# Kernel optimization log

Measured on AMD Instinct MI355X. Metric: run time of the kernel, lower is better.

The kernel has to match this reference:

```python
import jax, jax.numpy as jnp
import numpy as np

N_NODES = 50000
N_EDGES = 1600000
IN_DIM = 6
HID = 128
OUT = 128
N_LAYERS = 3
N_EXPERTS = 4
N_GRAPHS = 16
LOGN_SCALE = float(np.log(1e4))  # normalizes log(graph size) into ~[0,1]


def setup_inputs() -> dict:
    key = jax.random.key(0)
    ks = jax.random.split(key, 10)
    x = jax.random.normal(ks[0], (N_NODES, IN_DIM), dtype=jnp.float32)
    edge_index = jax.random.randint(ks[1], (2, N_EDGES), 0, N_NODES, dtype=jnp.int64)
    batch = jnp.sort(jax.random.randint(ks[2], (N_NODES,), 0, N_GRAPHS, dtype=jnp.int64))
    s = 1.0 / np.sqrt(HID)
    W_enc = jax.random.normal(ks[3], (IN_DIM, HID), dtype=jnp.float32) / np.sqrt(IN_DIM)
    b_enc = jnp.zeros((HID,), dtype=jnp.float32)
    # per-expert, per-layer GraphConv weights (hidden->hidden ... hidden->out; dims equal here)
    W_self = jax.random.normal(ks[4], (N_EXPERTS, N_LAYERS, HID, OUT), dtype=jnp.float32) * s
    W_nbr = jax.random.normal(ks[5], (N_EXPERTS, N_LAYERS, HID, OUT), dtype=jnp.float32) * s
    b_conv = jnp.zeros((N_EXPERTS, N_LAYERS, OUT), dtype=jnp.float32)
    centers = jnp.linspace(0.0, 1.0, N_EXPERTS, dtype=jnp.float32)
    return {"x": x, "edge_index": edge_index, "batch": batch, "W_enc": W_enc,
            "b_enc": b_enc, "W_self": W_self, "W_nbr": W_nbr, "b_conv": b_conv,
            "centers": centers}


def _expert(h, src, dst, Ws, Wn, b):
    # Ws, Wn: [L, H, H]; b: [L, H]
    for l in range(N_LAYERS):
        agg = jax.ops.segment_sum(h[src], dst, num_segments=N_NODES)  # gather+scatter
        h = h @ Ws[l] + agg @ Wn[l] + b[l]
        if l < N_LAYERS - 1:
            h = jax.nn.relu(h)
    return h


def reference(x, edge_index, batch, W_enc, b_enc, W_self, W_nbr, b_conv, centers):
    src, dst = edge_index[0], edge_index[1]
    h = jax.nn.relu(x @ W_enc + b_enc)  # SharedBusEncoder
    # graph size features: normalized log(#nodes per graph), per node
    counts = jax.ops.segment_sum(jnp.ones((N_NODES,), jnp.float32), batch,
                                 num_segments=N_GRAPHS)
    logn = jnp.log(jnp.maximum(counts, 1.0))[batch] / LOGN_SCALE  # [N]
    probs = jax.nn.softmax(-(logn[:, None] - centers[None, :]) ** 2, axis=-1)  # [N, E]
    y = jax.vmap(_expert, in_axes=(None, None, None, 0, 0, 0))(
        h, src, dst, W_self, W_nbr, b_conv)  # [E, N, OUT]
    return jnp.einsum('enh,ne->nh', y, probs)
```

## Files before the change

kernel.cpp:

```cpp
#include <hip/hip_runtime.h>

#define NN 50000
#define NE 1600000
#define NG 16
#define HID 128
#define NEXP 4
#define LOGN_SCALE 9.210340371976184f

#define NBUK 256
#define NPB  196
#define NBLK 128
#define EPB  ((NE + NBLK - 1)/NBLK)
#define MAXB 16384

typedef unsigned short u16;
typedef unsigned int u32;
typedef unsigned char u8;
typedef __attribute__((ext_vector_type(8))) short short8b;
typedef __attribute__((ext_vector_type(4))) float f32x4;
typedef __attribute__((ext_vector_type(2))) float f32x2;

static __device__ __forceinline__ float bf2f(u16 u){
  union { u32 i; float f; } c; c.i = ((u32)u)<<16; return c.f;
}
static __device__ __forceinline__ u16 f2bf(float f){
  union { float f; u32 i; } c; c.f = f;
  return (u16)((c.i + 0x7fffu + ((c.i>>16)&1u)) >> 16);
}
static __device__ __forceinline__ u8 f2fp8(float v){
  return (u8)(__builtin_amdgcn_cvt_pk_fp8_f32(v, v, 0, false) & 0xffu);
}

__global__ void k_bounds(const int* __restrict__ batch, int* __restrict__ gstart){
  int g = threadIdx.x;
  if(g > NG) return;
  int lo = 0, hi = NN;
  while(lo < hi){ int mid = (lo+hi)>>1; if(batch[mid] < g) lo = mid+1; else hi = mid; }
  gstart[g] = lo;
}

__global__ void k_probs(const int* __restrict__ batch, const int* __restrict__ gstart,
                        const float* __restrict__ centers, float* __restrict__ probs){
  int n = blockIdx.x*blockDim.x + threadIdx.x;
  if(n >= NN) return;
  int b = batch[n];
  float c = (float)(gstart[b+1] - gstart[b]);
  float logn = logf(fmaxf(c, 1.f)) * (1.f/LOGN_SCALE);
  float s[NEXP]; float m = -1e30f;
  #pragma unroll
  for(int e=0;e<NEXP;e++){ float d = logn - centers[e]; s[e] = -d*d; m = fmaxf(m, s[e]); }
  float sum = 0.f;
  #pragma unroll
  for(int e=0;e<NEXP;e++){ s[e] = expf(s[e]-m); sum += s[e]; }
  float inv = 1.f/sum;
  #pragma unroll
  for(int e=0;e<NEXP;e++) probs[n*NEXP+e] = s[e]*inv;
}

__global__ void k_enc(const float* __restrict__ x, const float* __restrict__ Wenc,
                      const float* __restrict__ benc, u16* __restrict__ h0,
                      u8* __restrict__ h08, float esc){
  int t = blockIdx.x*blockDim.x + threadIdx.x;
  if(t >= NN*HID) return;
  int n = t >> 7, j = t & 127;
  float acc = benc[j];
  #pragma unroll
  for(int k=0;k<6;k++) acc += x[n*6+k]*Wenc[k*HID+j];
  float v = fmaxf(acc, 0.f);
  h0[t] = f2bf(v);
  h08[t] = f2fp8(v*esc);
}

__global__ void k_wcvtT(const float* __restrict__ Wself, const float* __restrict__ Wnbr,
                        u16* __restrict__ WbfT){
  int t = blockIdx.x*blockDim.x + threadIdx.x;
  if(t >= 12*HID*256) return;
  int el = t / (HID*256);
  int r  = t % (HID*256);
  int j  = r >> 8;
  int k  = r & 255;
  float v = (k < HID) ? Wself[(size_t)el*HID*HID + (size_t)k*HID + j]
                      : Wnbr [(size_t)el*HID*HID + (size_t)(k-HID)*HID + j];
  WbfT[t] = f2bf(v);
}

__global__ __launch_bounds__(256) void k_hist(const int* __restrict__ dst,
                                              int* __restrict__ hist){
  __shared__ int h[NBUK];
  for(int i=threadIdx.x; i<NBUK; i+=256) h[i] = 0;
  __syncthreads();
  int e0 = blockIdx.x*EPB, e1 = min(NE, e0 + EPB);
  for(int e = e0 + (int)threadIdx.x; e < e1; e += 256)
    atomicAdd(&h[dst[e]/NPB], 1);
  __syncthreads();
  for(int i=threadIdx.x; i<NBUK; i+=256) hist[blockIdx.x*NBUK + i] = h[i];
}

__global__ __launch_bounds__(1024) void k_hscan(const int* __restrict__ hist,
                                                int* __restrict__ hoff,
                                                int* __restrict__ bbase){
  __shared__ int sd[NBLK*NBUK];
  __shared__ int ps[1024];
  int t = threadIdx.x;
  for(int i=t; i<NBLK*NBUK; i+=1024){
    int bucket = i >> 7;
    int blk = i & (NBLK-1);
    sd[i] = hist[blk*NBUK + bucket];
  }
  __syncthreads();
  int base = t*32, sum = 0;
  #pragma unroll
  for(int i=0;i<32;i++){ int v = sd[base+i]; sd[base+i] = sum; sum += v; }
  ps[t] = sum;
  __syncthreads();
  for(int d=1; d<1024; d<<=1){
    int v = (t>=d) ? ps[t-d] : 0;
    __syncthreads();
    ps[t] += v;
    __syncthreads();
  }
  int add = (t>0) ? ps[t-1] : 0;
  for(int i=base; i<base+32; i++){
    int bucket = i >> 7, blk = i & (NBLK-1);
    int v = sd[i] + add;
    hoff[blk*NBUK + bucket] = v;
    if(blk == 0) bbase[bucket] = v;
  }
  if(t == 1023) bbase[NBUK] = NE;
}

__global__ __launch_bounds__(256) void k_scatter(const int* __restrict__ src,
                                                 const int* __restrict__ dst,
                                                 const int* __restrict__ hoff,
                                                 u32* __restrict__ packed){
  __shared__ u32 ent[EPB];
  __shared__ u32 outp[EPB];
  __shared__ u32 cnt[NBUK], exc[NBUK], cur[NBUK], gb[NBUK];
  int t = threadIdx.x;
  int e0 = blockIdx.x*EPB;
  int len = min(EPB, NE - e0);
  cnt[t] = 0;
  __syncthreads();
  for(int i=t; i<len; i+=256){
    int d = dst[e0+i];
    u32 b = (u32)(d/NPB);
    ent[i] = (u32)src[e0+i] | ((u32)(d - (int)b*NPB) << 16) | (b << 24);
    atomicAdd(&cnt[b], 1u);
  }
  __syncthreads();
  u32 c = cnt[t];
  exc[t] = c;
  __syncthreads();
  for(int d=1; d<256; d<<=1){
    u32 v = (t>=(u32)d) ? exc[t-d] : 0u;
    __syncthreads();
    exc[t] += v;
    __syncthreads();
  }
  u32 excl = exc[t] - c;
  cur[t] = excl;
  gb[t] = (u32)hoff[blockIdx.x*NBUK + t];
  __syncthreads();
  exc[t] = excl;
  __syncthreads();
  for(int i=t; i<len; i+=256){
    u32 v = ent[i];
    u32 p = atomicAdd(&cur[v>>24], 1u);
    outp[p] = v;
  }
  __syncthreads();
  for(int i=t; i<len; i+=256){
    u32 v = outp[i];
    u32 b = v >> 24;
    packed[gb[b] + ((u32)i - exc[b])] = v & 0x00ffffffu;
  }
}

__global__ __launch_bounds__(256) void k_build(const u32* __restrict__ packed,
                                               const int* __restrict__ bbase,
                                               int* __restrict__ offs,
                                               u16* __restrict__ srcs16){
  __shared__ u32 ent[MAXB];
  __shared__ u16 outb[MAXB];
  __shared__ u32 cnt[256], exc[256], cur[256];
  int b = blockIdx.x, t = threadIdx.x;
  int e0 = bbase[b], e1 = bbase[b+1];
  int len = e1 - e0, cap = min(len, MAXB);
  for(int i=t; i<cap; i+=256) ent[i] = packed[e0+i];
  cnt[t] = 0;
  __syncthreads();
  for(int i=t; i<len; i+=256){
    u32 v = (i < MAXB) ? ent[i] : packed[e0+i];
    atomicAdd(&cnt[(v>>16)&0xffu], 1u);
  }
  __syncthreads();
  u32 c = cnt[t];
  exc[t] = c;
  __syncthreads();
  for(int d=1; d<256; d<<=1){
    u32 v = (t>=(u32)d) ? exc[t-d] : 0u;
    __syncthreads();
    exc[t] += v;
    __syncthreads();
  }
  u32 excl = exc[t] - c;
  int node = b*NPB + t;
  if(t < NPB && node < NN) offs[node] = e0 + (int)excl;
  cur[t] = excl;
  if(b == NBUK-1 && t == 0) offs[NN] = NE;
  __syncthreads();
  for(int i=t; i<len; i+=256){
    u32 v = (i < MAXB) ? ent[i] : packed[e0+i];
    u32 p = atomicAdd(&cur[(v>>16)&0xffu], 1u);
    u16 sv = (u16)(v & 0xffffu);
    if(p < (u32)MAXB) outb[p] = sv;
    else srcs16[e0+p] = sv;
  }
  __syncthreads();
  for(int i=t; i<cap; i+=256) srcs16[e0+i] = outb[i];
}

template<int BPL>
__global__ __launch_bounds__(256) void k_agg8(const u8* __restrict__ hin,
                                              const int* __restrict__ offs,
                                              const u16* __restrict__ srcs,
                                              u16* __restrict__ hout, float inv_scale){
  const int W = BPL*64;
  int node = blockIdx.x*4 + (threadIdx.x>>6);
  if(node >= NN) return;
  int lane = threadIdx.x & 63;
  const u8* hbase = hin + lane*BPL;
  float acc[BPL];
  #pragma unroll
  for(int i=0;i<BPL;i++) acc[i] = 0.f;
  int beg = offs[node], end = offs[node+1];
  for(int eb=beg; eb<end; eb+=64){
    int idx = eb + lane;
    int s = (idx < end) ? (int)srcs[idx] : 0;
    int cnt = min(64, end-eb);
    int j = 0;
    if(BPL == 8){
      for(; j+8<=cnt; j+=8){
        uint2 v[8];
        #pragma unroll
        for(int u=0;u<8;u++){
          int sj = __shfl(s, j+u, 64);
          v[u] = *(const uint2*)(hbase + (size_t)sj*W);
        }
        #pragma unroll
        for(int u=0;u<8;u++){
          f32x2 f0 = __builtin_amdgcn_cvt_pk_f32_fp8(v[u].x, false);
          f32x2 f1 = __builtin_amdgcn_cvt_pk_f32_fp8(v[u].x, true);
          f32x2 f2 = __builtin_amdgcn_cvt_pk_f32_fp8(v[u].y, false);
          f32x2 f3 = __builtin_amdgcn_cvt_pk_f32_fp8(v[u].y, true);
          acc[0]+=f0.x; acc[1]+=f0.y; acc[2]+=f1.x; acc[3]+=f1.y;
          acc[4]+=f2.x; acc[5]+=f2.y; acc[6]+=f3.x; acc[7]+=f3.y;
        }
      }
      for(; j<cnt; j++){
        int sj = __shfl(s, j, 64);
        uint2 v = *(const uint2*)(hbase + (size_t)sj*W);
        f32x2 f0 = __builtin_amdgcn_cvt_pk_f32_fp8(v.x, false);
        f32x2 f1 = __builtin_amdgcn_cvt_pk_f32_fp8(v.x, true);
        f32x2 f2 = __builtin_amdgcn_cvt_pk_f32_fp8(v.y, false);
        f32x2 f3 = __builtin_amdgcn_cvt_pk_f32_fp8(v.y, true);
        acc[0]+=f0.x; acc[1]+=f0.y; acc[2]+=f1.x; acc[3]+=f1.y;
        acc[4]+=f2.x; acc[5]+=f2.y; acc[6]+=f3.x; acc[7]+=f3.y;
      }
    } else {
      for(; j+8<=cnt; j+=8){
        u32 v[8];
        #pragma unroll
        for(int u=0;u<8;u++){
          int sj = __shfl(s, j+u, 64);
          v[u] = *(const u16*)(hbase + (size_t)sj*W);
        }
        #pragma unroll
        for(int u=0;u<8;u++){
          f32x2 f0 = __builtin_amdgcn_cvt_pk_f32_fp8(v[u], false);
          acc[0]+=f0.x; acc[1]+=f0.y;
        }
      }
      for(; j<cnt; j++){
        int sj = __shfl(s, j, 64);
        u32 v = *(const u16*)(hbase + (size_t)sj*W);
        f32x2 f0 = __builtin_amdgcn_cvt_pk_f32_fp8(v, false);
        acc[0]+=f0.x; acc[1]+=f0.y;
      }
    }
  }
  u16* o = hout + (size_t)node*W + lane*BPL;
  #pragma unroll
  for(int i=0;i<BPL;i++) o[i] = f2bf(acc[i]*inv_scale);
}

#define RPB 256
template<bool RELU>
__global__ __launch_bounds__(256) void k_gemm_mfma(
    const u16* __restrict__ hin, const u16* __restrict__ aggin,
    int in_stride, int in_eoff,
    const u16* __restrict__ WbfT, const float* __restrict__ bconv,
    int layer, u16* __restrict__ hout, u8* __restrict__ hout8, float enc8)
{
  int e = blockIdx.y;
  int wave = threadIdx.x >> 6, lane = threadIdx.x & 63;
  int l16 = lane & 15, lq = lane >> 4;
  int c0 = wave*32;
  const u16* WT = WbfT + (size_t)((e*3+layer)*HID)*256;

  short8b Bf[2][8];
  #pragma unroll
  for(int ct=0; ct<2; ct++){
    const u16* wp = WT + (size_t)(c0 + ct*16 + l16)*256 + lq*8;
    #pragma unroll
    for(int ks=0; ks<8; ks++)
      Bf[ct][ks] = *(const short8b*)(wp + ks*32);
  }
  const float* bias = bconv + (e*3+layer)*HID;
  float b0 = bias[c0 + l16], b1 = bias[c0 + 16 + l16];

  int nbase = blockIdx.x * RPB;
  #pragma unroll 1
  for(int it=0; it<RPB/32; it++){
    int n0 = nbase + it*32;
    if(n0 >= NN) break;
    f32x4 acc[2][2];
    #pragma unroll
    for(int rt=0; rt<2; rt++){
      acc[rt][0] = (f32x4){b0,b0,b0,b0};
      acc[rt][1] = (f32x4){b1,b1,b1,b1};
    }
    #pragma unroll
    for(int ks=0; ks<8; ks++){
      #pragma unroll
      for(int rt=0; rt<2; rt++){
        int n = n0 + rt*16 + l16;
        if(n > NN-1) n = NN-1;
        const u16* base = (ks < 4)
            ? (hin   + (size_t)n*in_stride + (size_t)e*in_eoff)
            : (aggin + (size_t)n*in_stride + (size_t)e*in_eoff - 128);
        short8b Af = *(const short8b*)(base + ks*32 + lq*8);
        acc[rt][0] = __builtin_amdgcn_mfma_f32_16x16x32_bf16(Af, Bf[0][ks], acc[rt][0], 0,0,0);
        acc[rt][1] = __builtin_amdgcn_mfma_f32_16x16x32_bf16(Af, Bf[1][ks], acc[rt][1], 0,0,0);
      }
    }
    #pragma unroll
    for(int rt=0; rt<2; rt++){
      int rowb = n0 + rt*16 + lq*4;
      #pragma unroll
      for(int r=0; r<4; r++){
        int n = rowb + r;
        if(n < NN){
          float v0 = acc[rt][0][r], v1 = acc[rt][1][r];
          if(RELU){ v0 = fmaxf(v0, 0.f); v1 = fmaxf(v1, 0.f); }
          u16* op = hout + (size_t)n*(NEXP*HID) + e*HID;
          op[c0 + l16]      = f2bf(v0);
          op[c0 + 16 + l16] = f2bf(v1);
          if(hout8){
            u8* op8 = hout8 + (size_t)n*(NEXP*HID) + e*HID;
            op8[c0 + l16]      = f2fp8(v0*enc8);
            op8[c0 + 16 + l16] = f2fp8(v1*enc8);
          }
        }
      }
    }
  }
}

__global__ void k_combine(const u16* __restrict__ y, const float* __restrict__ probs,
                          float* __restrict__ out){
  int t = blockIdx.x*blockDim.x + threadIdx.x;
  if(t >= NN*HID) return;
  int n = t >> 7, j = t & 127;
  const u16* yp = y + (size_t)n*(NEXP*HID);
  const float* pp = probs + n*NEXP;
  float r = pp[0]*bf2f(yp[j]) + pp[1]*bf2f(yp[HID+j])
          + pp[2]*bf2f(yp[2*HID+j]) + pp[3]*bf2f(yp[3*HID+j]);
  out[t] = r;
}

extern "C" void kernel_launch(void* const* d_in, const int* in_sizes, int n_in,
                              void* d_out, int out_size, void* d_ws, size_t ws_size,
                              hipStream_t stream){
  const float* x      = (const float*)d_in[0];
  const int*   eidx   = (const int*)d_in[1];
  const int*   batch  = (const int*)d_in[2];
  const float* Wenc   = (const float*)d_in[3];
  const float* benc   = (const float*)d_in[4];
  const float* Wself  = (const float*)d_in[5];
  const float* Wnbr   = (const float*)d_in[6];
  const float* bconv  = (const float*)d_in[7];
  const float* centers= (const float*)d_in[8];
  float* out = (float*)d_out;
  const int* src = eidx;
  const int* dst = eidx + NE;

  char* w = (char*)d_ws;
  size_t off = 0;
  auto alloc = [&](size_t b)->char*{ char* p = w + off; off = (off + b + 255) & ~(size_t)255; return p; };

  u16* h0    = (u16*)alloc((size_t)NN*HID*2);
  u16* agg0  = (u16*)alloc((size_t)NN*HID*2);
  u16* hA    = (u16*)alloc((size_t)NN*NEXP*HID*2);
  u16* hB    = (u16*)alloc((size_t)NN*NEXP*HID*2);
  u16* agg   = (u16*)alloc((size_t)NN*NEXP*HID*2);
  u16* WbfT  = (u16*)alloc((size_t)12*HID*256*2);
  u8*  h08   = (u8*)alloc((size_t)NN*HID);
  u8*  hA8   = (u8*)alloc((size_t)NN*NEXP*HID);
  float* probs = (float*)alloc((size_t)NN*NEXP*4);
  int* gstart = (int*)alloc(256);
  int* offs  = (int*)alloc((size_t)(NN+1)*4);
  u32* packed= (u32*)alloc((size_t)NE*4);
  u16* srcs16= (u16*)alloc((size_t)NE*2);
  int* hist  = (int*)alloc((size_t)NBLK*NBUK*4);
  int* hoff  = (int*)alloc((size_t)NBLK*NBUK*4);
  int* bbase = (int*)alloc((size_t)(NBUK+1)*4);
  if(off > ws_size) return;
  u8* hB8 = (u8*)h0;

  k_bounds<<<1, 32, 0, stream>>>(batch, gstart);
  k_probs<<<(NN+255)/256, 256, 0, stream>>>(batch, gstart, centers, probs);
  k_enc<<<(NN*HID+255)/256, 256, 0, stream>>>(x, Wenc, benc, h0, h08, 0.5f);
  k_wcvtT<<<(12*HID*256+255)/256, 256, 0, stream>>>(Wself, Wnbr, WbfT);

  k_hist<<<NBLK, 256, 0, stream>>>(dst, hist);
  k_hscan<<<1, 1024, 0, stream>>>(hist, hoff, bbase);
  k_scatter<<<NBLK, 256, 0, stream>>>(src, dst, hoff, packed);
  k_build<<<NBUK, 256, 0, stream>>>(packed, bbase, offs, srcs16);

  dim3 ggrid((NN + RPB - 1)/RPB, NEXP);

  k_agg8<2><<<(NN+3)/4, 256, 0, stream>>>(h08, offs, srcs16, agg0, 2.0f);
  k_gemm_mfma<true><<<ggrid, 256, 0, stream>>>(h0, agg0, HID, 0, WbfT, bconv, 0,
                                               hA, hA8, 1.f/16.f);
  k_agg8<8><<<(NN+3)/4, 256, 0, stream>>>(hA8, offs, srcs16, agg, 16.f);
  k_gemm_mfma<true><<<ggrid, 256, 0, stream>>>(hA, agg, NEXP*HID, HID, WbfT, bconv, 1,
                                               hB, hB8, 1.f/32.f);
  k_agg8<8><<<(NN+3)/4, 256, 0, stream>>>(hB8, offs, srcs16, agg, 32.f);
  k_gemm_mfma<false><<<ggrid, 256, 0, stream>>>(hB, agg, NEXP*HID, HID, WbfT, bconv, 2,
                                                hA, (u8*)nullptr, 0.f);

  k_combine<<<(NN*HID+255)/256, 256, 0, stream>>>(hA, probs, out);
}
```

Before: 611.9 us.

## Fuse aggregation, GEMM and expert combine into one kernel per layer

```diff
diff --git a/kernel.cpp b/kernel.cpp
--- a/kernel.cpp
+++ b/kernel.cpp
@@ -29,6 +29,18 @@
 }
 static __device__ __forceinline__ u8 f2fp8(float v){
   return (u8)(__builtin_amdgcn_cvt_pk_fp8_f32(v, v, 0, false) & 0xffu);
+}
+static __device__ __forceinline__ short8b fp8x8_to_bf16(uint2 v){
+  f32x2 a = __builtin_amdgcn_cvt_pk_f32_fp8(v.x, false);
+  f32x2 b = __builtin_amdgcn_cvt_pk_f32_fp8(v.x, true);
+  f32x2 c = __builtin_amdgcn_cvt_pk_f32_fp8(v.y, false);
+  f32x2 d = __builtin_amdgcn_cvt_pk_f32_fp8(v.y, true);
+  short8b t;
+  t[0]=(short)f2bf(a.x); t[1]=(short)f2bf(a.y);
+  t[2]=(short)f2bf(b.x); t[3]=(short)f2bf(b.y);
+  t[4]=(short)f2bf(c.x); t[5]=(short)f2bf(c.y);
+  t[6]=(short)f2bf(d.x); t[7]=(short)f2bf(d.y);
+  return t;
 }
 
 __global__ void k_bounds(const int* __restrict__ batch, int* __restrict__ gstart){
@@ -58,17 +70,14 @@
 }
 
 __global__ void k_enc(const float* __restrict__ x, const float* __restrict__ Wenc,
-                      const float* __restrict__ benc, u16* __restrict__ h0,
-                      u8* __restrict__ h08, float esc){
+                      const float* __restrict__ benc, u8* __restrict__ h08, float esc){
   int t = blockIdx.x*blockDim.x + threadIdx.x;
   if(t >= NN*HID) return;
   int n = t >> 7, j = t & 127;
   float acc = benc[j];
   #pragma unroll
   for(int k=0;k<6;k++) acc += x[n*6+k]*Wenc[k*HID+j];
-  float v = fmaxf(acc, 0.f);
-  h0[t] = f2bf(v);
-  h08[t] = f2fp8(v*esc);
+  h08[t] = f2fp8(fmaxf(acc, 0.f)*esc);
 }
 
 __global__ void k_wcvtT(const float* __restrict__ Wself, const float* __restrict__ Wnbr,
@@ -220,163 +229,219 @@
   for(int i=t; i<cap; i+=256) srcs16[e0+i] = outb[i];
 }
 
-template<int BPL>
-__global__ __launch_bounds__(256) void k_agg8(const u8* __restrict__ hin,
-                                              const int* __restrict__ offs,
-                                              const u16* __restrict__ srcs,
-                                              u16* __restrict__ hout, float inv_scale){
-  const int W = BPL*64;
-  int node = blockIdx.x*4 + (threadIdx.x>>6);
-  if(node >= NN) return;
-  int lane = threadIdx.x & 63;
-  const u8* hbase = hin + lane*BPL;
-  float acc[BPL];
-  #pragma unroll
-  for(int i=0;i<BPL;i++) acc[i] = 0.f;
-  int beg = offs[node], end = offs[node+1];
-  for(int eb=beg; eb<end; eb+=64){
-    int idx = eb + lane;
-    int s = (idx < end) ? (int)srcs[idx] : 0;
-    int cnt = min(64, end-eb);
-    int j = 0;
+template<int TW, bool RELU, bool LAST>
+__global__ __launch_bounds__(256) void k_fused(
+    const u8* __restrict__ tin, const int* __restrict__ offs,
+    const u16* __restrict__ srcs, const u16* __restrict__ WbfT,
+    const float* __restrict__ bconv, int layer,
+    const float* __restrict__ probs,
+    u8* __restrict__ tout, float* __restrict__ outp,
+    float bias_fold, float store_fold)
+{
+  constexpr int BPL = TW/64;
+  __shared__ u16 G[32*TW];
+  int wave = threadIdx.x>>6, lane = threadIdx.x&63;
+  int l16 = lane&15, lq = lane>>4;
+  int n0 = blockIdx.x*32;
+
+  const u8* hbase = tin + lane*BPL;
+  for(int i=0;i<8;i++){
+    int row = wave*8 + i;
+    int node = n0 + row;
+    float acc[BPL];
+    #pragma unroll
+    for(int b=0;b<BPL;b++) acc[b]=0.f;
+    if(node < NN){
+      int beg = offs[node], end = offs[node+1];
+      for(int eb=beg; eb<end; eb+=64){
+        int idx = eb + lane;
+        int s = (idx < end) ? (int)srcs[idx] : 0;
+        int cnt = min(64, end-eb);
+        int j = 0;
+        if(BPL == 8){
+          for(; j+8<=cnt; j+=8){
+            uint2 v[8];
+            #pragma unroll
+            for(int u=0;u<8;u++){
+              int sj = __shfl(s, j+u, 64);
+              v[u] = *(const uint2*)(hbase + (size_t)sj*TW);
+            }
+            #pragma unroll
+            for(int u=0;u<8;u++){
+              f32x2 f0 = __builtin_amdgcn_cvt_pk_f32_fp8(v[u].x, false);
+              f32x2 f1 = __builtin_amdgcn_cvt_pk_f32_fp8(v[u].x, true);
+              f32x2 f2 = __builtin_amdgcn_cvt_pk_f32_fp8(v[u].y, false);
+              f32x2 f3 = __builtin_amdgcn_cvt_pk_f32_fp8(v[u].y, true);
+              acc[0]+=f0.x; acc[1]+=f0.y; acc[2]+=f1.x; acc[3]+=f1.y;
+              acc[4]+=f2.x; acc[5]+=f2.y; acc[6]+=f3.x; acc[7]+=f3.y;
+            }
+          }
+          for(; j<cnt; j++){
+            int sj = __shfl(s, j, 64);
+            uint2 v = *(const uint2*)(hbase + (size_t)sj*TW);
+            f32x2 f0 = __builtin_amdgcn_cvt_pk_f32_fp8(v.x, false);
+            f32x2 f1 = __builtin_amdgcn_cvt_pk_f32_fp8(v.x, true);
+            f32x2 f2 = __builtin_amdgcn_cvt_pk_f32_fp8(v.y, false);
+            f32x2 f3 = __builtin_amdgcn_cvt_pk_f32_fp8(v.y, true);
+            acc[0]+=f0.x; acc[1]+=f0.y; acc[2]+=f1.x; acc[3]+=f1.y;
+            acc[4]+=f2.x; acc[5]+=f2.y; acc[6]+=f3.x; acc[7]+=f3.y;
+          }
+        } else {
+          for(; j+8<=cnt; j+=8){
+            u32 v[8];
+            #pragma unroll
+            for(int u=0;u<8;u++){
+              int sj = __shfl(s, j+u, 64);
+              v[u] = *(const u16*)(hbase + (size_t)sj*TW);
+            }
+            #pragma unroll
+            for(int u=0;u<8;u++){
+              f32x2 f0 = __builtin_amdgcn_cvt_pk_f32_fp8(v[u], false);
+              acc[0]+=f0.x; acc[1]+=f0.y;
+            }
+          }
+          for(; j<cnt; j++){
+            int sj = __shfl(s, j, 64);
+            u32 v = *(const u16*)(hbase + (size_t)sj*TW);
+            f32x2 f0 = __builtin_amdgcn_cvt_pk_f32_fp8(v, false);
+            acc[0]+=f0.x; acc[1]+=f0.y;
+          }
+        }
+      }
+    }
+    u32 boff = (u32)(lane*BPL*2) ^ (u32)((row&7)<<4);
+    u16* gp = (u16*)((char*)G + (size_t)row*(TW*2) + boff);
     if(BPL == 8){
-      for(; j+8<=cnt; j+=8){
-        uint2 v[8];
-        #pragma unroll
-        for(int u=0;u<8;u++){
-          int sj = __shfl(s, j+u, 64);
-          v[u] = *(const uint2*)(hbase + (size_t)sj*W);
-        }
-        #pragma unroll
-        for(int u=0;u<8;u++){
-          f32x2 f0 = __builtin_amdgcn_cvt_pk_f32_fp8(v[u].x, false);
-          f32x2 f1 = __builtin_amdgcn_cvt_pk_f32_fp8(v[u].x, true);
-          f32x2 f2 = __builtin_amdgcn_cvt_pk_f32_fp8(v[u].y, false);
-          f32x2 f3 = __builtin_amdgcn_cvt_pk_f32_fp8(v[u].y, true);
-          acc[0]+=f0.x; acc[1]+=f0.y; acc[2]+=f1.x; acc[3]+=f1.y;
-          acc[4]+=f2.x; acc[5]+=f2.y; acc[6]+=f3.x; acc[7]+=f3.y;
-        }
-      }
-      for(; j<cnt; j++){
-        int sj = __shfl(s, j, 64);
-        uint2 v = *(const uint2*)(hbase + (size_t)sj*W);
-        f32x2 f0 = __builtin_amdgcn_cvt_pk_f32_fp8(v.x, false);
-        f32x2 f1 = __builtin_amdgcn_cvt_pk_f32_fp8(v.x, true);
-        f32x2 f2 = __builtin_amdgcn_cvt_pk_f32_fp8(v.y, false);
-        f32x2 f3 = __builtin_amdgcn_cvt_pk_f32_fp8(v.y, true);
-        acc[0]+=f0.x; acc[1]+=f0.y; acc[2]+=f1.x; acc[3]+=f1.y;
-        acc[4]+=f2.x; acc[5]+=f2.y; acc[6]+=f3.x; acc[7]+=f3.y;
-      }
+      short8b tv;
+      #pragma unroll
+      for(int b=0;b<8;b++) tv[b] = (short)f2bf(acc[b]);
+      *(short8b*)gp = tv;
     } else {
-      for(; j+8<=cnt; j+=8){
-        u32 v[8];
-        #pragma unroll
-        for(int u=0;u<8;u++){
-          int sj = __shfl(s, j+u, 64);
-          v[u] = *(const u16*)(hbase + (size_t)sj*W);
-        }
-        #pragma unroll
-        for(int u=0;u<8;u++){
-          f32x2 f0 = __builtin_amdgcn_cvt_pk_f32_fp8(v[u], false);
-          acc[0]+=f0.x; acc[1]+=f0.y;
-        }
-      }
-      for(; j<cnt; j++){
-        int sj = __shfl(s, j, 64);
-        u32 v = *(const u16*)(hbase + (size_t)sj*W);
-        f32x2 f0 = __builtin_amdgcn_cvt_pk_f32_fp8(v, false);
-        acc[0]+=f0.x; acc[1]+=f0.y;
-      }
-    }
-  }
-  u16* o = hout + (size_t)node*W + lane*BPL;
-  #pragma unroll
-  for(int i=0;i<BPL;i++) o[i] = f2bf(acc[i]*inv_scale);
-}
-
-#define RPB 256
-template<bool RELU>
-__global__ __launch_bounds__(256) void k_gemm_mfma(
-    const u16* __restrict__ hin, const u16* __restrict__ aggin,
-    int in_stride, int in_eoff,
-    const u16* __restrict__ WbfT, const float* __restrict__ bconv,
-    int layer, u16* __restrict__ hout, u8* __restrict__ hout8, float enc8)
-{
-  int e = blockIdx.y;
-  int wave = threadIdx.x >> 6, lane = threadIdx.x & 63;
-  int l16 = lane & 15, lq = lane >> 4;
-  int c0 = wave*32;
-  const u16* WT = WbfT + (size_t)((e*3+layer)*HID)*256;
-
-  short8b Bf[2][8];
-  #pragma unroll
-  for(int ct=0; ct<2; ct++){
-    const u16* wp = WT + (size_t)(c0 + ct*16 + l16)*256 + lq*8;
-    #pragma unroll
-    for(int ks=0; ks<8; ks++)
-      Bf[ct][ks] = *(const short8b*)(wp + ks*32);
-  }
-  const float* bias = bconv + (e*3+layer)*HID;
-  float b0 = bias[c0 + l16], b1 = bias[c0 + 16 + l16];
-
-  int nbase = blockIdx.x * RPB;
-  #pragma unroll 1
-  for(int it=0; it<RPB/32; it++){
-    int n0 = nbase + it*32;
-    if(n0 >= NN) break;
-    f32x4 acc[2][2];
+      gp[0] = f2bf(acc[0]); gp[1] = f2bf(acc[1]);
+    }
+  }
+  __syncthreads();
+
+  if(!LAST){
+    int e = wave;
+    const u16* WT = WbfT + (size_t)((e*3+layer)*HID)*256;
+    const int eoff = (TW==512) ? e*128 : 0;
+    short8b Af[2][8];
     #pragma unroll
     for(int rt=0; rt<2; rt++){
-      acc[rt][0] = (f32x4){b0,b0,b0,b0};
-      acc[rt][1] = (f32x4){b1,b1,b1,b1};
-    }
-    #pragma unroll
-    for(int ks=0; ks<8; ks++){
+      int n = n0 + rt*16 + l16; if(n > NN-1) n = NN-1;
+      const u8* srow = tin + (size_t)n*TW;
+      #pragma unroll
+      for(int ks=0; ks<4; ks++)
+        Af[rt][ks] = fp8x8_to_bf16(*(const uint2*)(srow + eoff + ks*32 + lq*8));
+      int row = rt*16 + l16;
+      #pragma unroll
+      for(int ks=4; ks<8; ks++){
+        u32 boff = (u32)((eoff + (ks-4)*32 + lq*8)*2) ^ (u32)((row&7)<<4);
+        Af[rt][ks] = *(const short8b*)((char*)G + (size_t)row*(TW*2) + boff);
+      }
+    }
+    const float* bias = bconv + (e*3+layer)*HID;
+    #pragma unroll 1
+    for(int ct=0; ct<8; ct++){
+      f32x4 binit = *(const f32x4*)(bias + ct*16 + lq*4);
+      f32x4 acc0, acc1;
+      #pragma unroll
+      for(int r=0;r<4;r++){ acc0[r] = binit[r]*bias_fold; acc1[r] = acc0[r]; }
+      const u16* wp = WT + (size_t)(ct*16 + l16)*256 + lq*8;
+      #pragma unroll
+      for(int ks=0; ks<8; ks++){
+        short8b Bf = *(const short8b*)(wp + ks*32);
+        acc0 = __builtin_amdgcn_mfma_f32_16x16x32_bf16(Bf, Af[0][ks], acc0, 0,0,0);
+        acc1 = __builtin_amdgcn_mfma_f32_16x16x32_bf16(Bf, Af[1][ks], acc1, 0,0,0);
+      }
       #pragma unroll
       for(int rt=0; rt<2; rt++){
         int n = n0 + rt*16 + l16;
-        if(n > NN-1) n = NN-1;
-        const u16* base = (ks < 4)
-            ? (hin   + (size_t)n*in_stride + (size_t)e*in_eoff)
-            : (aggin + (size_t)n*in_stride + (size_t)e*in_eoff - 128);
-        short8b Af = *(const short8b*)(base + ks*32 + lq*8);
-        acc[rt][0] = __builtin_amdgcn_mfma_f32_16x16x32_bf16(Af, Bf[0][ks], acc[rt][0], 0,0,0);
-        acc[rt][1] = __builtin_amdgcn_mfma_f32_16x16x32_bf16(Af, Bf[1][ks], acc[rt][1], 0,0,0);
+        if(n < NN){
+          f32x4 a = rt ? acc1 : acc0;
+          float v0,v1,v2,v3;
+          if(RELU){
+            v0=fmaxf(a[0],0.f)*store_fold; v1=fmaxf(a[1],0.f)*store_fold;
+            v2=fmaxf(a[2],0.f)*store_fold; v3=fmaxf(a[3],0.f)*store_fold;
+          } else {
+            v0=a[0]*store_fold; v1=a[1]*store_fold; v2=a[2]*store_fold; v3=a[3]*store_fold;
+          }
+          u32 wv = __builtin_amdgcn_cvt_pk_fp8_f32(v0, v1, 0, false);
+          wv = __builtin_amdgcn_cvt_pk_fp8_f32(v2, v3, wv, true);
+          *(u32*)(tout + (size_t)n*512 + e*128 + ct*16 + lq*4) = wv;
+        }
+      }
+    }
+  } else {
+    f32x4 tot[2][2];
+    #pragma unroll
+    for(int rt=0;rt<2;rt++){
+      #pragma unroll
+      for(int ct=0;ct<2;ct++){
+        #pragma unroll
+        for(int r=0;r<4;r++) tot[rt][ct][r] = 0.f;
+      }
+    }
+    float pv[2][4];
+    #pragma unroll
+    for(int rt=0;rt<2;rt++){
+      int n = n0 + rt*16 + l16; if(n > NN-1) n = NN-1;
+      #pragma unroll
+      for(int e=0;e<4;e++) pv[rt][e] = probs[n*NEXP + e];
+    }
+    #pragma unroll 1
+    for(int e=0;e<4;e++){
+      const u16* WT = WbfT + (size_t)((e*3+layer)*HID)*256;
+      const int eoff = e*128;
+      short8b Af[2][8];
+      #pragma unroll
+      for(int rt=0; rt<2; rt++){
+        int n = n0 + rt*16 + l16; if(n > NN-1) n = NN-1;
+        const u8* srow = tin + (size_t)n*TW;
+        #pragma unroll
+        for(int ks=0; ks<4; ks++)
+          Af[rt][ks] = fp8x8_to_bf16(*(const uint2*)(srow + eoff + ks*32 + lq*8));
+        int row = rt*16 + l16;
+        #pragma unroll
+        for(int ks=4; ks<8; ks++){
+          u32 boff = (u32)((eoff + (ks-4)*32 + lq*8)*2) ^ (u32)((row&7)<<4);
+          Af[rt][ks] = *(const short8b*)((char*)G + (size_t)row*(TW*2) + boff);
+        }
+      }
+      const float* bias = bconv + (e*3+layer)*HID;
+      #pragma unroll
+      for(int ct=0; ct<2; ct++){
+        int cb = wave*32 + ct*16;
+        f32x4 binit = *(const f32x4*)(bias + cb + lq*4);
+        f32x4 acc0, acc1;
+        #pragma unroll
+        for(int r=0;r<4;r++){ acc0[r] = binit[r]*bias_fold; acc1[r] = acc0[r]; }
+        const u16* wp = WT + (size_t)(cb + l16)*256 + lq*8;
+        #pragma unroll
+        for(int ks=0; ks<8; ks++){
+          short8b Bf = *(const short8b*)(wp + ks*32);
+          acc0 = __builtin_amdgcn_mfma_f32_16x16x32_bf16(Bf, Af[0][ks], acc0, 0,0,0);
+          acc1 = __builtin_amdgcn_mfma_f32_16x16x32_bf16(Bf, Af[1][ks], acc1, 0,0,0);
+        }
+        float s0 = pv[0][e]*store_fold, s1 = pv[1][e]*store_fold;
+        #pragma unroll
+        for(int r=0;r<4;r++){
+          tot[0][ct][r] += s0*acc0[r];
+          tot[1][ct][r] += s1*acc1[r];
+        }
       }
     }
     #pragma unroll
     for(int rt=0; rt<2; rt++){
-      int rowb = n0 + rt*16 + lq*4;
-      #pragma unroll
-      for(int r=0; r<4; r++){
-        int n = rowb + r;
-        if(n < NN){
-          float v0 = acc[rt][0][r], v1 = acc[rt][1][r];
-          if(RELU){ v0 = fmaxf(v0, 0.f); v1 = fmaxf(v1, 0.f); }
-          u16* op = hout + (size_t)n*(NEXP*HID) + e*HID;
-          op[c0 + l16]      = f2bf(v0);
-          op[c0 + 16 + l16] = f2bf(v1);
-          if(hout8){
-            u8* op8 = hout8 + (size_t)n*(NEXP*HID) + e*HID;
-            op8[c0 + l16]      = f2fp8(v0*enc8);
-            op8[c0 + 16 + l16] = f2fp8(v1*enc8);
-          }
-        }
-      }
-    }
-  }
-}
-
-__global__ void k_combine(const u16* __restrict__ y, const float* __restrict__ probs,
-                          float* __restrict__ out){
-  int t = blockIdx.x*blockDim.x + threadIdx.x;
-  if(t >= NN*HID) return;
-  int n = t >> 7, j = t & 127;
-  const u16* yp = y + (size_t)n*(NEXP*HID);
-  const float* pp = probs + n*NEXP;
-  float r = pp[0]*bf2f(yp[j]) + pp[1]*bf2f(yp[HID+j])
-          + pp[2]*bf2f(yp[2*HID+j]) + pp[3]*bf2f(yp[3*HID+j]);
-  out[t] = r;
+      int n = n0 + rt*16 + l16;
+      if(n < NN){
+        #pragma unroll
+        for(int ct=0; ct<2; ct++)
+          *(f32x4*)(outp + (size_t)n*HID + wave*32 + ct*16 + lq*4) = tot[rt][ct];
+      }
+    }
+  }
 }
 
 extern "C" void kernel_launch(void* const* d_in, const int* in_sizes, int n_in,
@@ -399,14 +464,10 @@
   size_t off = 0;
   auto alloc = [&](size_t b)->char*{ char* p = w + off; off = (off + b + 255) & ~(size_t)255; return p; };
 
-  u16* h0    = (u16*)alloc((size_t)NN*HID*2);
-  u16* agg0  = (u16*)alloc((size_t)NN*HID*2);
-  u16* hA    = (u16*)alloc((size_t)NN*NEXP*HID*2);
-  u16* hB    = (u16*)alloc((size_t)NN*NEXP*HID*2);
-  u16* agg   = (u16*)alloc((size_t)NN*NEXP*HID*2);
-  u16* WbfT  = (u16*)alloc((size_t)12*HID*256*2);
   u8*  h08   = (u8*)alloc((size_t)NN*HID);
   u8*  hA8   = (u8*)alloc((size_t)NN*NEXP*HID);
+  u8*  hB8   = (u8*)alloc((size_t)NN*NEXP*HID);
+  u16* WbfT  = (u16*)alloc((size_t)12*HID*256*2);
   float* probs = (float*)alloc((size_t)NN*NEXP*4);
   int* gstart = (int*)alloc(256);
   int* offs  = (int*)alloc((size_t)(NN+1)*4);
@@ -416,11 +477,10 @@
   int* hoff  = (int*)alloc((size_t)NBLK*NBUK*4);
   int* bbase = (int*)alloc((size_t)(NBUK+1)*4);
   if(off > ws_size) return;
-  u8* hB8 = (u8*)h0;
 
   k_bounds<<<1, 32, 0, stream>>>(batch, gstart);
   k_probs<<<(NN+255)/256, 256, 0, stream>>>(batch, gstart, centers, probs);
-  k_enc<<<(NN*HID+255)/256, 256, 0, stream>>>(x, Wenc, benc, h0, h08, 0.5f);
+  k_enc<<<(NN*HID+255)/256, 256, 0, stream>>>(x, Wenc, benc, h08, 0.5f);
   k_wcvtT<<<(12*HID*256+255)/256, 256, 0, stream>>>(Wself, Wnbr, WbfT);
 
   k_hist<<<NBLK, 256, 0, stream>>>(dst, hist);
@@ -428,17 +488,11 @@
   k_scatter<<<NBLK, 256, 0, stream>>>(src, dst, hoff, packed);
   k_build<<<NBUK, 256, 0, stream>>>(packed, bbase, offs, srcs16);
 
-  dim3 ggrid((NN + RPB - 1)/RPB, NEXP);
-
-  k_agg8<2><<<(NN+3)/4, 256, 0, stream>>>(h08, offs, srcs16, agg0, 2.0f);
-  k_gemm_mfma<true><<<ggrid, 256, 0, stream>>>(h0, agg0, HID, 0, WbfT, bconv, 0,
-                                               hA, hA8, 1.f/16.f);
-  k_agg8<8><<<(NN+3)/4, 256, 0, stream>>>(hA8, offs, srcs16, agg, 16.f);
-  k_gemm_mfma<true><<<ggrid, 256, 0, stream>>>(hA, agg, NEXP*HID, HID, WbfT, bconv, 1,
-                                               hB, hB8, 1.f/32.f);
-  k_agg8<8><<<(NN+3)/4, 256, 0, stream>>>(hB8, offs, srcs16, agg, 32.f);
-  k_gemm_mfma<false><<<ggrid, 256, 0, stream>>>(hB, agg, NEXP*HID, HID, WbfT, bconv, 2,
-                                                hA, (u8*)nullptr, 0.f);
-
-  k_combine<<<(NN*HID+255)/256, 256, 0, stream>>>(hA, probs, out);
-}
+  int nblocks = (NN + 31)/32;
+  k_fused<128,true,false><<<nblocks, 256, 0, stream>>>(
+      h08, offs, srcs16, WbfT, bconv, 0, nullptr, hA8, nullptr, 0.5f, 0.125f);
+  k_fused<512,true,false><<<nblocks, 256, 0, stream>>>(
+      hA8, offs, srcs16, WbfT, bconv, 1, nullptr, hB8, nullptr, 0.0625f, 0.5f);
+  k_fused<512,false,true><<<nblocks, 256, 0, stream>>>(
+      hB8, offs, srcs16, WbfT, bconv, 2, probs, nullptr, out, 0.03125f, 32.0f);
+}
```

Result: faster. 570.1 us (-6.8%).
